# Kernel optimization log

Hardware: AMD Instinct MI355X
Metric: run time of the kernel (lower is better)

The kernel has to match this reference:

```python
import jax, jax.numpy as jnp
import numpy as np

_SAMPLING_EPS = 1e-05
_RMAX = 0.9999999403953552          # largest float32 uniform from tl.rand
_RMAX_LOG = -5.960464477539063e-08  # log(_RMAX)


def setup_inputs() -> dict:
    key = jax.random.key(0)
    k1, k2, k3, k4, k5 = jax.random.split(key, 5)
    B, V = 256, 128000
    logits = jax.random.normal(k1, (B, V), dtype=jnp.float32) * 4.0
    temperature = jax.random.uniform(k2, (B,), dtype=jnp.float32, minval=0.1, maxval=1.5)
    top_k = jax.random.randint(k3, (B,), 1, 1000).astype(jnp.int32)
    top_p = jax.random.uniform(k4, (B,), dtype=jnp.float32, minval=0.5, maxval=1.0)
    gumbel_u = jax.random.uniform(k5, (B, V), dtype=jnp.float32)
    return {
        "logits": logits,
        "temperature": temperature,
        "top_k": top_k,
        "top_p": top_p,
        "gumbel_u": gumbel_u,
        "num_logprobs": 20,
    }


def reference(logits, temperature, top_k, top_p, gumbel_u, num_logprobs):
    B, V = logits.shape
    # --- apply_temperature: divide by temp, temp<eps treated as 1.0 (greedy) ---
    temp = jnp.where(temperature < _SAMPLING_EPS, 1.0, temperature)
    logits = logits.astype(jnp.float32) / temp[:, None]

    # --- apply_top_k_top_p: sort ascending, mask, scatter back ---
    idx_sort = jnp.argsort(logits, axis=-1)                      # ascending
    logits_sort = jnp.take_along_axis(logits, idx_sort, axis=-1)
    # top-k: value of the k-th largest is at position V-k in ascending order
    k_pos = (V - top_k.astype(jnp.int32))[:, None]
    thresh = jnp.take_along_axis(logits_sort, k_pos, axis=-1)    # [B,1]
    logits_sort = jnp.where(logits_sort < thresh, -jnp.inf, logits_sort)
    # top-p: drop ascending prefix whose cumulative prob <= 1-p (keep last)
    probs_sort = jax.nn.softmax(logits_sort, axis=-1)
    cum = jnp.cumsum(probs_sort, axis=-1)
    mask_p = cum <= (1.0 - top_p)[:, None]
    mask_p = mask_p.at[:, -1].set(False)
    logits_sort = jnp.where(mask_p, -jnp.inf, logits_sort)
    # unsort back to vocab order
    inv = jnp.argsort(idx_sort, axis=-1)
    logits_f = jnp.take_along_axis(logits_sort, inv, axis=-1)

    # --- softmax + gumbel-trick sampling: argmax(p / -log(u)) ---
    probs = jax.nn.softmax(logits_f, axis=-1)
    q = -jnp.where(gumbel_u >= _RMAX, _RMAX_LOG, jnp.log(gumbel_u))
    greedy = (temperature < _SAMPLING_EPS)[:, None]  # kernel skips these rows
    ratio = jnp.where(greedy, probs, probs / q)
    sampled = jnp.argmax(ratio, axis=-1)             # [B]

    # --- gather_logprobs ---
    logprobs = jax.nn.log_softmax(logits_f, axis=-1)
    sampled_lp = jnp.take_along_axis(logprobs, sampled[:, None], axis=-1)  # [B,1]
    ranks = jnp.sum(logprobs > sampled_lp, axis=-1)                        # [B]
    topk_lp, topk_idx = jax.lax.top_k(logprobs, num_logprobs)
    indices = jnp.concatenate([sampled[:, None], topk_idx], axis=1)        # [B,1+K]
    lp_vals = jnp.concatenate([sampled_lp, topk_lp], axis=1)               # [B,1+K]

    return sampled[:, None], indices, lp_vals, ranks
```

## Files before the change

kernel.cpp:

```cpp
#include <hip/hip_runtime.h>
#include <math.h>

#define NTHR 1024
#define CAP 8192
#define BINS 4096
#define SMALL 1024
#define GUARD 16u
#define SS 4096

#define RMAX_F 0.9999999403953552f
#define RMAX_LOG_F -5.960464477539063e-08f
#define NEG_BIG -3.0e38f

__device__ __forceinline__ unsigned keyOf(float v) {
    unsigned b = __float_as_uint(v);
    return (b & 0x80000000u) ? ~b : (b | 0x80000000u);
}
__device__ __forceinline__ float valOfKey(unsigned k) {
    unsigned b = (k & 0x80000000u) ? (k ^ 0x80000000u) : ~k;
    return __uint_as_float(b);
}
__device__ __forceinline__ unsigned long long shflXor64(unsigned long long v, int m) {
    int lo = __shfl_xor((int)(unsigned)v, m);
    int hi = __shfl_xor((int)(unsigned)(v >> 32), m);
    return ((unsigned long long)(unsigned)hi << 32) | (unsigned)lo;
}

__global__ __launch_bounds__(NTHR) void sampler_kernel(
    const float* __restrict__ logits,
    const float* __restrict__ temperature,
    const int* __restrict__ top_kv,
    const float* __restrict__ top_pv,
    const float* __restrict__ gumbel,
    float* __restrict__ out,
    int B, int V, int K)
{
    const int r = blockIdx.x;
    const int tid = threadIdx.x;
    const int lane = tid & 63;
    const int wid = tid >> 6;

    __shared__ unsigned long long cand[CAP];
    __shared__ unsigned long long cand2[SMALL];
    __shared__ unsigned refHist[16 * 257];
    __shared__ int wtotI[16];
    __shared__ float varr[1024];
    __shared__ float Earr[1024];
    __shared__ float sfx[1024];
    __shared__ float sfx2[1024];
    __shared__ unsigned char flagArr[1024];
    __shared__ unsigned bitmap[64];
    __shared__ unsigned s_prefix;
    __shared__ int s_cntgt, s_total, s_lvl;
    __shared__ int s_ncand, s_nc2, s_nkeep, s_rank, s_g0, s_g1;
    __shared__ unsigned long long s_amax;
    __shared__ float s_vs;

    unsigned* hist = (unsigned*)cand;

    const float* row = logits + (long long)r * V;
    const float* urow = gumbel + (long long)r * V;

    float traw = temperature[r];
    bool greedy = traw < 1e-5f;
    float t = greedy ? 1.0f : traw;
    int k = top_kv[r];
    if (k < 1) k = 1;
    if (k > V) k = V;
    float p = top_pv[r];

    const float4* row4 = (const float4*)row;
    const int V4 = V >> 2;
    const int Vt = V4 << 2;
    const unsigned cpy = tid & 1u;

#define H4(v4) do { \
        atomicAdd(&hist[((keyOf((v4).x) >> 20) << 1) | cpy], 1u); \
        atomicAdd(&hist[((keyOf((v4).y) >> 20) << 1) | cpy], 1u); \
        atomicAdd(&hist[((keyOf((v4).z) >> 20) << 1) | cpy], 1u); \
        atomicAdd(&hist[((keyOf((v4).w) >> 20) << 1) | cpy], 1u); \
    } while (0)
#define SPEC1(val, gidx_, thr_) do { \
        float _v = (val); \
        if (_v >= (thr_)) { \
            int _pos = atomicAdd(&s_ncand, 1); \
            if (_pos < CAP) \
                cand[_pos] = ((unsigned long long)keyOf(_v) << 32) | (unsigned)(~(unsigned)(gidx_)); \
        } \
    } while (0)

    for (int i = tid; i < BINS * 2; i += NTHR) hist[i] = 0;
    __syncthreads();
    {
        int f4pos = (int)(((long long)tid * V4) >> 10);
        float4 sv = row4[f4pos];
        H4(sv);
    }
    __syncthreads();
    int ts;
    {
        int tc = 2 * k + 400;
        if (tc > 2400) tc = 2400;
        if (tc < 600) tc = 600;
        ts = (int)(((long long)tc * SS + V - 1) / V);
        if (ts < 4) ts = 4;
    }
    {
        int base = tid << 2;
        int cs = 0;
        #pragma unroll
        for (int j = 0; j < 4; ++j)
            cs += (int)(hist[(base + j) * 2] + hist[(base + j) * 2 + 1]);
        int vv = cs;
        #pragma unroll
        for (int d = 1; d < 64; d <<= 1) {
            int o = __shfl_down(vv, d);
            if (lane + d < 64) vv += o;
        }
        if (lane == 0) wtotI[wid] = vv;
        __syncthreads();
        int off = 0;
        for (int w = wid + 1; w < 16; ++w) off += wtotI[w];
        int mine = vv + off;
        int above = mine - cs;
        if (mine >= ts && above < ts) {
            int run = above;
            for (int b = base + 3; b >= base; --b) {
                int mb = (int)(hist[b * 2] + hist[b * 2 + 1]);
                if (run + mb >= ts) { s_prefix = (unsigned)b; break; }
                run += mb;
            }
        }
        if (tid == 0) s_ncand = 0;
        __syncthreads();
    }
    unsigned tlo = s_prefix << 20;
    float thrF = valOfKey(tlo);

    {
        int i = tid;
        for (; i + 3 * NTHR < V4; i += 4 * NTHR) {
            float4 a = row4[i];
            float4 b = row4[i + NTHR];
            float4 c = row4[i + 2 * NTHR];
            float4 d = row4[i + 3 * NTHR];
            SPEC1(a.x, i * 4 + 0, thrF); SPEC1(a.y, i * 4 + 1, thrF);
            SPEC1(a.z, i * 4 + 2, thrF); SPEC1(a.w, i * 4 + 3, thrF);
            SPEC1(b.x, (i + NTHR) * 4 + 0, thrF); SPEC1(b.y, (i + NTHR) * 4 + 1, thrF);
            SPEC1(b.z, (i + NTHR) * 4 + 2, thrF); SPEC1(b.w, (i + NTHR) * 4 + 3, thrF);
            SPEC1(c.x, (i + 2 * NTHR) * 4 + 0, thrF); SPEC1(c.y, (i + 2 * NTHR) * 4 + 1, thrF);
            SPEC1(c.z, (i + 2 * NTHR) * 4 + 2, thrF); SPEC1(c.w, (i + 2 * NTHR) * 4 + 3, thrF);
            SPEC1(d.x, (i + 3 * NTHR) * 4 + 0, thrF); SPEC1(d.y, (i + 3 * NTHR) * 4 + 1, thrF);
            SPEC1(d.z, (i + 3 * NTHR) * 4 + 2, thrF); SPEC1(d.w, (i + 3 * NTHR) * 4 + 3, thrF);
        }
        for (; i < V4; i += NTHR) {
            float4 a = row4[i];
            SPEC1(a.x, i * 4 + 0, thrF); SPEC1(a.y, i * 4 + 1, thrF);
            SPEC1(a.z, i * 4 + 2, thrF); SPEC1(a.w, i * 4 + 3, thrF);
        }
        for (int ii = Vt + tid; ii < V; ii += NTHR)
            SPEC1(row[ii], ii, thrF);
    }
    __syncthreads();
    int ncand = s_ncand;
    const bool fastok = (ncand >= k && ncand <= CAP);

    if (!fastok) {
        for (int i = tid; i < BINS * 2; i += NTHR) hist[i] = 0;
        __syncthreads();
        {
            int i = tid;
            for (; i + 3 * NTHR < V4; i += 4 * NTHR) {
                float4 a = row4[i];
                float4 b = row4[i + NTHR];
                float4 c = row4[i + 2 * NTHR];
                float4 d = row4[i + 3 * NTHR];
                H4(a); H4(b); H4(c); H4(d);
            }
            for (; i < V4; i += NTHR) { float4 a = row4[i]; H4(a); }
            for (int ii = Vt + tid; ii < V; ii += NTHR)
                atomicAdd(&hist[((keyOf(row[ii]) >> 20) << 1) | cpy], 1u);
        }
        __syncthreads();
        {
            int base = tid << 2;
            int cs = 0;
            #pragma unroll
            for (int j = 0; j < 4; ++j)
                cs += (int)(hist[(base + j) * 2] + hist[(base + j) * 2 + 1]);
            int vv = cs;
            #pragma unroll
            for (int d = 1; d < 64; d <<= 1) {
                int o = __shfl_down(vv, d);
                if (lane + d < 64) vv += o;
            }
            if (lane == 0) wtotI[wid] = vv;
            __syncthreads();
            int off = 0;
            for (int w = wid + 1; w < 16; ++w) off += wtotI[w];
            int mine = vv + off;
            int above = mine - cs;
            if (mine >= k && above < k) {
                int run = above;
                for (int b = base + 3; b >= base; --b) {
                    int mb = (int)(hist[b * 2] + hist[b * 2 + 1]);
                    if (run + mb >= k) {
                        s_prefix = (unsigned)b; s_cntgt = run; s_total = run + mb; s_lvl = 0;
                        break;
                    }
                    run += mb;
                }
            }
        }
        for (int level = 1; level <= 2; ++level) {
            __syncthreads();
            if (s_total <= CAP) break;
            for (int i = tid; i < 512; i += NTHR) hist[i] = 0;
            __syncthreads();
            unsigned pfx = s_prefix;
            const int msh = 32 - (12 + 8 * (level - 1));
            const int bsh = msh - 8;
            for (int i = tid; i < V4; i += NTHR) {
                float4 l4 = row4[i];
                float vv4[4] = { l4.x, l4.y, l4.z, l4.w };
                #pragma unroll
                for (int j = 0; j < 4; ++j) {
                    unsigned key = keyOf(vv4[j]);
                    if ((key >> msh) == pfx)
                        atomicAdd(&hist[(((key >> bsh) & 255u) << 1) | cpy], 1u);
                }
            }
            for (int i = Vt + tid; i < V; i += NTHR) {
                unsigned key = keyOf(row[i]);
                if ((key >> msh) == pfx)
                    atomicAdd(&hist[(((key >> bsh) & 255u) << 1) | cpy], 1u);
            }
            __syncthreads();
            if (tid == 0) {
                int run = s_cntgt;
                for (int b = 255; b >= 0; --b) {
                    int mb = (int)(hist[b * 2] + hist[b * 2 + 1]);
                    if (run + mb >= k) {
                        s_prefix = (pfx << 8) | (unsigned)b; s_cntgt = run; s_total = run + mb;
                        break;
                    }
                    run += mb;
                }
                s_lvl = level;
            }
        }
        __syncthreads();
        tlo = s_prefix << (20 - 8 * s_lvl);
        thrF = valOfKey(tlo);
        if (tid == 0) s_ncand = 0;
        __syncthreads();
        {
            int i = tid;
            for (; i + 3 * NTHR < V4; i += 4 * NTHR) {
                float4 a = row4[i];
                float4 b = row4[i + NTHR];
                float4 c = row4[i + 2 * NTHR];
                float4 d = row4[i + 3 * NTHR];
                SPEC1(a.x, i * 4 + 0, thrF); SPEC1(a.y, i * 4 + 1, thrF);
                SPEC1(a.z, i * 4 + 2, thrF); SPEC1(a.w, i * 4 + 3, thrF);
                SPEC1(b.x, (i + NTHR) * 4 + 0, thrF); SPEC1(b.y, (i + NTHR) * 4 + 1, thrF);
                SPEC1(b.z, (i + NTHR) * 4 + 2, thrF); SPEC1(b.w, (i + NTHR) * 4 + 3, thrF);
                SPEC1(c.x, (i + 2 * NTHR) * 4 + 0, thrF); SPEC1(c.y, (i + 2 * NTHR) * 4 + 1, thrF);
                SPEC1(c.z, (i + 2 * NTHR) * 4 + 2, thrF); SPEC1(c.w, (i + 2 * NTHR) * 4 + 3, thrF);
                SPEC1(d.x, (i + 3 * NTHR) * 4 + 0, thrF); SPEC1(d.y, (i + 3 * NTHR) * 4 + 1, thrF);
                SPEC1(d.z, (i + 3 * NTHR) * 4 + 2, thrF); SPEC1(d.w, (i + 3 * NTHR) * 4 + 3, thrF);
            }
            for (; i < V4; i += NTHR) {
                float4 a = row4[i];
                SPEC1(a.x, i * 4 + 0, thrF); SPEC1(a.y, i * 4 + 1, thrF);
                SPEC1(a.z, i * 4 + 2, thrF); SPEC1(a.w, i * 4 + 3, thrF);
            }
            for (int ii = Vt + tid; ii < V; ii += NTHR)
                SPEC1(row[ii], ii, thrF);
        }
        __syncthreads();
        ncand = s_ncand;
        if (ncand > CAP) ncand = CAP;
        if (k > ncand) k = ncand;
    }
    if (k > ncand) k = ncand;

    bool fromC2 = false;
    bool bigSort = false;
    if (ncand > SMALL) {
        unsigned pfx; int run; int bb;
        if (fastok) { pfx = 0u; run = 0; bb = 32; }
        else { pfx = s_prefix; run = s_cntgt; bb = 20 - 8 * s_lvl; }
        int totR = ncand;
        while (totR > SMALL - 16 && bb > 0) {
            int step = (bb >= 8) ? 8 : bb;
            bb -= step;
            int nbins = 1 << step;
            for (int i = tid; i < 16 * 257; i += NTHR) refHist[i] = 0;
            __syncthreads();
            {
                const int sh = bb + step;
                const unsigned lc = (unsigned)(lane & 15) * 257u;
                for (int i = tid; i < ncand; i += NTHR) {
                    unsigned key = (unsigned)(cand[i] >> 32);
                    bool in = (sh >= 32) || ((key >> sh) == pfx);
                    if (in)
                        atomicAdd(&refHist[lc + ((key >> bb) & (unsigned)(nbins - 1))], 1u);
                }
            }
            __syncthreads();
            int cnt = 0;
            if (tid < 256 && tid < nbins) {
                #pragma unroll
                for (int c = 0; c < 16; ++c) cnt += (int)refHist[c * 257 + tid];
            }
            int vv = cnt;
            #pragma unroll
            for (int d = 1; d < 64; d <<= 1) {
                int o = __shfl_down(vv, d);
                if (lane + d < 64) vv += o;
            }
            if (tid < 256 && lane == 0) wtotI[wid] = vv;
            __syncthreads();
            if (tid < 256) {
                int off = 0;
                for (int w = wid + 1; w < 4; ++w) off += wtotI[w];
                int incl = vv + off;
                int abv = incl - cnt;
                int kk = k - run;
                if (incl >= kk && abv < kk) {
                    s_prefix = (pfx << step) | (unsigned)tid;
                    s_cntgt = run + abv;
                    s_total = run + abv + cnt;
                }
            }
            __syncthreads();
            pfx = s_prefix;
            run = s_cntgt;
            totR = s_total;
        }
        unsigned tref0 = (bb > 0) ? (pfx << bb) : pfx;
        unsigned tref = (tref0 >= GUARD) ? (tref0 - GUARD) : 0u;
        if (tid == 0) s_nc2 = 0;
        __syncthreads();
        for (int i = tid; i < ncand; i += NTHR) {
            unsigned long long cv = cand[i];
            bool pred = ((unsigned)(cv >> 32) >= tref);
            unsigned long long mask = __ballot(pred ? 1 : 0);
            if (mask) {
                int leader = __ffsll(mask) - 1;
                int cnt2 = __popcll(mask);
                int bpos = 0;
                if (lane == leader) bpos = atomicAdd(&s_nc2, cnt2);
                bpos = __shfl(bpos, leader);
                if (pred) {
                    int pos = bpos + __popcll(mask & ((1ULL << lane) - 1ULL));
                    if (pos < SMALL) cand2[pos] = cv;
                }
            }
        }
        __syncthreads();
        int nc2 = s_nc2;
        if (nc2 <= SMALL) { ncand = nc2; fromC2 = true; }
        else bigSort = true;
    }

    if (!bigSort) {
        const unsigned long long* src = fromC2 ? cand2 : cand;
        unsigned long long v = (tid < ncand) ? src[tid] : 0ULL;
        int seg = 0;
        #pragma unroll
        for (int size = 2; size <= SMALL; size <<= 1) {
            #pragma unroll
            for (int stride = size >> 1; stride > 0; stride >>= 1) {
                unsigned long long o;
                if (stride < 64) {
                    o = shflXor64(v, stride);
                } else {
                    cand[seg * SMALL + tid] = v;
                    __syncthreads();
                    o = cand[seg * SMALL + (tid ^ stride)];
                    seg ^= 1;
                }
                bool takeMax = (((tid & size) == 0) == ((tid & stride) == 0));
                unsigned long long mx = (v > o) ? v : o;
                unsigned long long mn = (v > o) ? o : v;
                v = takeMax ? mx : mn;
            }
        }
        cand[tid] = v;
        varr[tid] = (tid < ncand) ? (valOfKey((unsigned)(v >> 32)) / t) : NEG_BIG;
        __syncthreads();
    } else {
        int P = 2; while (P < ncand) P <<= 1;
        for (int i = ncand + tid; i < P; i += NTHR) cand[i] = 0ULL;
        __syncthreads();
        for (int size = 2; size <= P; size <<= 1) {
            for (int stride = size >> 1; stride > 0; stride >>= 1) {
                for (int i = tid; i < P; i += NTHR) {
                    int j = i ^ stride;
                    if (j > i) {
                        unsigned long long a = cand[i], b = cand[j];
                        bool up = ((i & size) == 0);
                        bool sw = up ? (a < b) : (a > b);
                        if (sw) { cand[i] = b; cand[j] = a; }
                    }
                }
                __syncthreads();
            }
        }
        for (int i = tid; i < 1024; i += NTHR)
            varr[i] = (i < ncand) ? (valOfKey((unsigned)(cand[i] >> 32)) / t) : NEG_BIG;
        __syncthreads();
    }

    const float m = varr[0];
    const float tkeyV = varr[k - 1];
    int ntop = k;
    while (ntop < ncand) {
        float vi = (ntop < 1024) ? varr[ntop]
                                 : (valOfKey((unsigned)(cand[ntop] >> 32)) / t);
        if (vi != tkeyV) break;
        ++ntop;
    }
    if (ntop > 1024) ntop = 1024;

    {
        float e = (tid < ntop) ? expf(varr[tid] - m) : 0.0f;
        Earr[tid] = e;
        sfx[tid] = e;
        if (tid == 0) { s_nkeep = 0; s_rank = 0; s_amax = 0ULL; }
        if (tid < 64) bitmap[tid] = 0;
    }
    __syncthreads();
    {
        float* A = sfx;
        float* Bf = sfx2;
        #pragma unroll
        for (int d = 1; d < 1024; d <<= 1) {
            float t0 = (tid + d < 1024) ? A[tid + d] : 0.0f;
            Bf[tid] = A[tid] + t0;
            __syncthreads();
            float* tmp = A; A = Bf; Bf = tmp;
        }
    }
    const float Zp = sfx[0];
    const float cmp = 1.0f - p;
    {
        int local = 0;
        for (int i = tid; i < ntop; i += NTHR)
            if (sfx[i] / Zp > cmp) local++;
        #pragma unroll
        for (int d = 1; d < 64; d <<= 1) local += __shfl_xor(local, d);
        if (lane == 0 && local) atomicAdd(&s_nkeep, local);
    }
    __syncthreads();
    const int nkeep = s_nkeep;
    if (tid == 0) {
        float vb = varr[nkeep - 1];
        int g0 = nkeep - 1;
        while (g0 > 0 && varr[g0 - 1] == vb) --g0;
        int g1 = nkeep;
        while (g1 < ntop && varr[g1] == vb) ++g1;
        s_g0 = g0; s_g1 = g1;
    }
    __syncthreads();
    const int g0 = s_g0, g1 = s_g1;
    const int mkeep = nkeep - g0;
    for (int i = g0 + tid; i < g1; i += NTHR) {
        unsigned gi = ~(unsigned)(cand[i] & 0xFFFFFFFFull);
        int rk = 0;
        for (int j = g0; j < g1; ++j) {
            unsigned gj = ~(unsigned)(cand[j] & 0xFFFFFFFFull);
            if (gj > gi) rk++;
        }
        flagArr[i] = (rk < mkeep) ? 1 : 0;
    }
    __syncthreads();

    const float Z2 = (nkeep < 1024) ? (Zp - sfx[nkeep]) : Zp;
    const float L = logf(Z2);

    {
        unsigned long long lm = 0ULL;
        for (int i = tid; i < g1; i += NTHR) {
            if (i < g0 || flagArr[i]) {
                unsigned lo = (unsigned)(cand[i] & 0xFFFFFFFFull);
                unsigned gidx = ~lo;
                float u = urow[gidx];
                float q = -((u >= RMAX_F) ? RMAX_LOG_F : logf(u));
                float prob = Earr[i] / Z2;
                float ratio = greedy ? prob : (prob / q);
                unsigned long long comp = ((unsigned long long)__float_as_uint(ratio) << 32) | lo;
                if (comp > lm) lm = comp;
                if (gidx < 2048) atomicOr(&bitmap[gidx >> 5], 1u << (gidx & 31));
            }
        }
        #pragma unroll
        for (int d = 1; d < 64; d <<= 1) {
            unsigned long long o = shflXor64(lm, d);
            if (o > lm) lm = o;
        }
        if (lane == 0 && lm) atomicMax(&s_amax, lm);
    }
    __syncthreads();
    const unsigned samp_lo = (unsigned)(s_amax & 0xFFFFFFFFull);
    const unsigned samp = ~samp_lo;
    for (int i = tid; i < ntop; i += NTHR)
        if ((unsigned)(cand[i] & 0xFFFFFFFFull) == samp_lo) s_vs = varr[i];
    __syncthreads();
    const float lp_s = (s_vs - m) - L;
    {
        int local = 0;
        for (int i = tid; i < nkeep; i += NTHR)
            if ((varr[i] - m) - L > lp_s) local++;
        #pragma unroll
        for (int d = 1; d < 64; d <<= 1) local += __shfl_xor(local, d);
        if (lane == 0 && local) atomicAdd(&s_rank, local);
    }
    __syncthreads();

    float* o_samp = out;
    float* o_idx  = out + B;
    float* o_lp   = out + B + (long long)B * (K + 1);
    float* o_rank = out + B + 2LL * B * (K + 1);
    const long long rowo = (long long)r * (K + 1);
    const int ntk = (nkeep < K) ? nkeep : K;

    if (tid < g1) {
        const int i = tid;
        bool kept = (i < g0) || flagArr[i];
        if (kept) {
            float v = varr[i];
            int rs, re, base;
            if (i >= g0) { rs = g0; re = g1; base = g0; }
            else {
                rs = i; while (rs > 0 && varr[rs - 1] == v) --rs;
                re = i + 1; while (re < g1 && varr[re] == v) ++re;
                base = rs;
            }
            if (base < ntk) {
                unsigned myidx = ~(unsigned)(cand[i] & 0xFFFFFFFFull);
                int cnt = 0;
                for (int j = rs; j < re; ++j) {
                    if (j == i) continue;
                    if (j >= g0 && !flagArr[j]) continue;
                    unsigned gj = ~(unsigned)(cand[j] & 0xFFFFFFFFull);
                    if (gj < myidx) cnt++;
                }
                int slot = base + cnt;
                if (slot < ntk) {
                    o_idx[rowo + 1 + slot] = (float)myidx;
                    o_lp[rowo + 1 + slot] = (v - m) - L;
                }
            }
        }
    }

    if (tid == 0) {
        o_samp[r] = (float)samp;
        o_idx[rowo] = (float)samp;
        o_lp[rowo] = lp_s;
        o_rank[r] = (float)s_rank;
        if (nkeep < K) {
            int j = 0;
            for (int c = nkeep; c < K; ++c) {
                while (bitmap[j >> 5] & (1u << (j & 31))) ++j;
                o_idx[rowo + 1 + c] = (float)j;
                o_lp[rowo + 1 + c] = NEG_BIG;
                ++j;
            }
        }
    }
}

extern "C" void kernel_launch(void* const* d_in, const int* in_sizes, int n_in,
                              void* d_out, int out_size, void* d_ws, size_t ws_size,
                              hipStream_t stream) {
    const float* logits      = (const float*)d_in[0];
    const float* temperature = (const float*)d_in[1];
    const int*   top_k       = (const int*)d_in[2];
    const float* top_p       = (const float*)d_in[3];
    const float* gumbel      = (const float*)d_in[4];
    int B = in_sizes[1];
    int V = in_sizes[0] / B;
    int K = (out_size / B - 4) / 2;
    sampler_kernel<<<B, NTHR, 0, stream>>>(logits, temperature, top_k, top_p,
                                           gumbel, (float*)d_out, B, V, K);
}
```

Measured before the change: 265.4 us.

## Split sampler into threshold, multi-block compaction, and tail kernels via workspace

Breaks the single per-row kernel into three launches. One estimates the candidate threshold from a sample, the next compacts candidates with four 256-thread blocks per row using global atomics into a workspace, and the last loads those candidates into LDS to finish selection and sampling. The aim is more parallelism in the full-row scan, which was bound to one 1024-thread block per row with very large LDS use and therefore low occupancy. In exchange it adds launch overhead, global atomics and a workspace round-trip, and it needs a large workspace (B*8192*8 bytes); if that is not provided, it falls back to the old single-kernel path.

New measurement: 622.8 us. +134.6%, slower.

```diff
diff --git a/kernel.cpp b/kernel.cpp
--- a/kernel.cpp
+++ b/kernel.cpp
@@ -7,10 +7,14 @@
 #define SMALL 1024
 #define GUARD 16u
 #define SS 4096
+#define NS 4
+#define ATHR 256
 
 #define RMAX_F 0.9999999403953552f
 #define RMAX_LOG_F -5.960464477539063e-08f
 #define NEG_BIG -3.0e38f
+
+typedef unsigned long long ull;
 
 __device__ __forceinline__ unsigned keyOf(float v) {
     unsigned b = __float_as_uint(v);
@@ -20,28 +24,167 @@
     unsigned b = (k & 0x80000000u) ? (k ^ 0x80000000u) : ~k;
     return __uint_as_float(b);
 }
-__device__ __forceinline__ unsigned long long shflXor64(unsigned long long v, int m) {
+__device__ __forceinline__ ull shflXor64(ull v, int m) {
     int lo = __shfl_xor((int)(unsigned)v, m);
     int hi = __shfl_xor((int)(unsigned)(v >> 32), m);
-    return ((unsigned long long)(unsigned)hi << 32) | (unsigned)lo;
+    return ((ull)(unsigned)hi << 32) | (unsigned)lo;
 }
 
-__global__ __launch_bounds__(NTHR) void sampler_kernel(
+
+#define H4(v4) do { \
+        atomicAdd(&hist[((keyOf((v4).x) >> 20) << 1) | cpy], 1u); \
+        atomicAdd(&hist[((keyOf((v4).y) >> 20) << 1) | cpy], 1u); \
+        atomicAdd(&hist[((keyOf((v4).z) >> 20) << 1) | cpy], 1u); \
+        atomicAdd(&hist[((keyOf((v4).w) >> 20) << 1) | cpy], 1u); \
+    } while (0)
+
+__global__ __launch_bounds__(NTHR) void a0_thresh(
+    const float* __restrict__ logits,
+    const int* __restrict__ top_kv,
+    int* __restrict__ ws_cnt,
+    unsigned* __restrict__ ws_tlo,
+    int B, int V)
+{
+    const int r = blockIdx.x;
+    const int tid = threadIdx.x;
+    const int lane = tid & 63;
+    const int wid = tid >> 6;
+    __shared__ unsigned hist[BINS * 2];
+    __shared__ int wtotI[16];
+    __shared__ unsigned s_prefix;
+
+    const float* row = logits + (long long)r * V;
+    const float4* row4 = (const float4*)row;
+    const int V4 = V >> 2;
+    const unsigned cpy = tid & 1u;
+
+    int k = top_kv[r];
+    if (k < 1) k = 1;
+    if (k > V) k = V;
+
+    for (int i = tid; i < BINS * 2; i += NTHR) hist[i] = 0;
+    __syncthreads();
+    {
+        int f4pos = (int)(((long long)tid * V4) >> 10);
+        float4 sv = row4[f4pos];
+        H4(sv);
+    }
+    __syncthreads();
+    int ts;
+    {
+        int tc = 2 * k + 400;
+        if (tc > 2400) tc = 2400;
+        if (tc < 600) tc = 600;
+        ts = (int)(((long long)tc * SS + V - 1) / V);
+        if (ts < 4) ts = 4;
+    }
+    {
+        int base = tid << 2;
+        int cs = 0;
+        #pragma unroll
+        for (int j = 0; j < 4; ++j)
+            cs += (int)(hist[(base + j) * 2] + hist[(base + j) * 2 + 1]);
+        int vv = cs;
+        #pragma unroll
+        for (int d = 1; d < 64; d <<= 1) {
+            int o = __shfl_down(vv, d);
+            if (lane + d < 64) vv += o;
+        }
+        if (lane == 0) wtotI[wid] = vv;
+        __syncthreads();
+        int off = 0;
+        for (int w = wid + 1; w < 16; ++w) off += wtotI[w];
+        int mine = vv + off;
+        int above = mine - cs;
+        if (mine >= ts && above < ts) {
+            int run = above;
+            for (int b = base + 3; b >= base; --b) {
+                int mb = (int)(hist[b * 2] + hist[b * 2 + 1]);
+                if (run + mb >= ts) { s_prefix = (unsigned)b; break; }
+                run += mb;
+            }
+        }
+    }
+    __syncthreads();
+    if (tid == 0) {
+        ws_tlo[r] = s_prefix << 20;
+        ws_cnt[r] = 0;
+    }
+}
+
+__global__ __launch_bounds__(ATHR) void a1_compact(
+    const float* __restrict__ logits,
+    const unsigned* __restrict__ ws_tlo,
+    int* __restrict__ ws_cnt,
+    ull* __restrict__ ws_cand,
+    int B, int V)
+{
+    const int r = blockIdx.x / NS;
+    const int s = blockIdx.x % NS;
+    const int tid = threadIdx.x;
+
+    const float* row = logits + (long long)r * V;
+    const float4* row4 = (const float4*)row;
+    const int V4 = V >> 2;
+    const int Vt = V4 << 2;
+    const float thrF = valOfKey(ws_tlo[r]);
+    int* cnt = ws_cnt + r;
+    ull* wc = ws_cand + (size_t)r * CAP;
+
+#define SPECG(val, gidx_) do { \
+        float _v = (val); \
+        if (_v >= thrF) { \
+            int _pos = atomicAdd(cnt, 1); \
+            if (_pos < CAP) \
+                wc[_pos] = ((ull)keyOf(_v) << 32) | (unsigned)(~(unsigned)(gidx_)); \
+        } \
+    } while (0)
+
+    const int q0 = (int)(((long long)s * V4) / NS);
+    const int q1 = (int)(((long long)(s + 1) * V4) / NS);
+    int i = q0 + tid;
+    for (; i + 3 * ATHR < q1; i += 4 * ATHR) {
+        float4 a = row4[i];
+        float4 b = row4[i + ATHR];
+        float4 c = row4[i + 2 * ATHR];
+        float4 d = row4[i + 3 * ATHR];
+        SPECG(a.x, i * 4 + 0); SPECG(a.y, i * 4 + 1);
+        SPECG(a.z, i * 4 + 2); SPECG(a.w, i * 4 + 3);
+        SPECG(b.x, (i + ATHR) * 4 + 0); SPECG(b.y, (i + ATHR) * 4 + 1);
+        SPECG(b.z, (i + ATHR) * 4 + 2); SPECG(b.w, (i + ATHR) * 4 + 3);
+        SPECG(c.x, (i + 2 * ATHR) * 4 + 0); SPECG(c.y, (i + 2 * ATHR) * 4 + 1);
+        SPECG(c.z, (i + 2 * ATHR) * 4 + 2); SPECG(c.w, (i + 2 * ATHR) * 4 + 3);
+        SPECG(d.x, (i + 3 * ATHR) * 4 + 0); SPECG(d.y, (i + 3 * ATHR) * 4 + 1);
+        SPECG(d.z, (i + 3 * ATHR) * 4 + 2); SPECG(d.w, (i + 3 * ATHR) * 4 + 3);
+    }
+    for (; i < q1; i += ATHR) {
+        float4 a = row4[i];
+        SPECG(a.x, i * 4 + 0); SPECG(a.y, i * 4 + 1);
+        SPECG(a.z, i * 4 + 2); SPECG(a.w, i * 4 + 3);
+    }
+    if (s == NS - 1)
+        for (int ii = Vt + tid; ii < V; ii += ATHR)
+            SPECG(row[ii], ii);
+}
+
+__global__ __launch_bounds__(NTHR) void sampler_tail(
     const float* __restrict__ logits,
     const float* __restrict__ temperature,
     const int* __restrict__ top_kv,
     const float* __restrict__ top_pv,
     const float* __restrict__ gumbel,
     float* __restrict__ out,
-    int B, int V, int K)
+    const int* __restrict__ ws_cnt,
+    const ull* __restrict__ ws_cand,
+    int B, int V, int K, int use_ws)
 {
     const int r = blockIdx.x;
     const int tid = threadIdx.x;
     const int lane = tid & 63;
     const int wid = tid >> 6;
 
-    __shared__ unsigned long long cand[CAP];
-    __shared__ unsigned long long cand2[SMALL];
+    __shared__ ull cand[CAP];
+    __shared__ ull cand2[SMALL];
     __shared__ unsigned refHist[16 * 257];
     __shared__ int wtotI[16];
     __shared__ float varr[1024];
@@ -53,7 +196,7 @@
     __shared__ unsigned s_prefix;
     __shared__ int s_cntgt, s_total, s_lvl;
     __shared__ int s_ncand, s_nc2, s_nkeep, s_rank, s_g0, s_g1;
-    __shared__ unsigned long long s_amax;
+    __shared__ ull s_amax;
     __shared__ float s_vs;
 
     unsigned* hist = (unsigned*)cand;
@@ -74,114 +217,48 @@
     const int Vt = V4 << 2;
     const unsigned cpy = tid & 1u;
 
-#define H4(v4) do { \
-        atomicAdd(&hist[((keyOf((v4).x) >> 20) << 1) | cpy], 1u); \
-        atomicAdd(&hist[((keyOf((v4).y) >> 20) << 1) | cpy], 1u); \
-        atomicAdd(&hist[((keyOf((v4).z) >> 20) << 1) | cpy], 1u); \
-        atomicAdd(&hist[((keyOf((v4).w) >> 20) << 1) | cpy], 1u); \
-    } while (0)
 #define SPEC1(val, gidx_, thr_) do { \
         float _v = (val); \
         if (_v >= (thr_)) { \
             int _pos = atomicAdd(&s_ncand, 1); \
             if (_pos < CAP) \
-                cand[_pos] = ((unsigned long long)keyOf(_v) << 32) | (unsigned)(~(unsigned)(gidx_)); \
+                cand[_pos] = ((ull)keyOf(_v) << 32) | (unsigned)(~(unsigned)(gidx_)); \
         } \
     } while (0)
 
-    for (int i = tid; i < BINS * 2; i += NTHR) hist[i] = 0;
-    __syncthreads();
-    {
-        int f4pos = (int)(((long long)tid * V4) >> 10);
-        float4 sv = row4[f4pos];
-        H4(sv);
-    }
-    __syncthreads();
-    int ts;
-    {
-        int tc = 2 * k + 400;
-        if (tc > 2400) tc = 2400;
-        if (tc < 600) tc = 600;
-        ts = (int)(((long long)tc * SS + V - 1) / V);
-        if (ts < 4) ts = 4;
-    }
-    {
-        int base = tid << 2;
-        int cs = 0;
-        #pragma unroll
-        for (int j = 0; j < 4; ++j)
-            cs += (int)(hist[(base + j) * 2] + hist[(base + j) * 2 + 1]);
-        int vv = cs;
-        #pragma unroll
-        for (int d = 1; d < 64; d <<= 1) {
-            int o = __shfl_down(vv, d);
-            if (lane + d < 64) vv += o;
-        }
-        if (lane == 0) wtotI[wid] = vv;
-        __syncthreads();
-        int off = 0;
-        for (int w = wid + 1; w < 16; ++w) off += wtotI[w];
-        int mine = vv + off;
-        int above = mine - cs;
-        if (mine >= ts && above < ts) {
-            int run = above;
-            for (int b = base + 3; b >= base; --b) {
-                int mb = (int)(hist[b * 2] + hist[b * 2 + 1]);
-                if (run + mb >= ts) { s_prefix = (unsigned)b; break; }
-                run += mb;
-            }
-        }
-        if (tid == 0) s_ncand = 0;
-        __syncthreads();
-    }
-    unsigned tlo = s_prefix << 20;
-    float thrF = valOfKey(tlo);
-
-    {
-        int i = tid;
-        for (; i + 3 * NTHR < V4; i += 4 * NTHR) {
-            float4 a = row4[i];
-            float4 b = row4[i + NTHR];
-            float4 c = row4[i + 2 * NTHR];
-            float4 d = row4[i + 3 * NTHR];
-            SPEC1(a.x, i * 4 + 0, thrF); SPEC1(a.y, i * 4 + 1, thrF);
-            SPEC1(a.z, i * 4 + 2, thrF); SPEC1(a.w, i * 4 + 3, thrF);
-            SPEC1(b.x, (i + NTHR) * 4 + 0, thrF); SPEC1(b.y, (i + NTHR) * 4 + 1, thrF);
-            SPEC1(b.z, (i + NTHR) * 4 + 2, thrF); SPEC1(b.w, (i + NTHR) * 4 + 3, thrF);
-            SPEC1(c.x, (i + 2 * NTHR) * 4 + 0, thrF); SPEC1(c.y, (i + 2 * NTHR) * 4 + 1, thrF);
-            SPEC1(c.z, (i + 2 * NTHR) * 4 + 2, thrF); SPEC1(c.w, (i + 2 * NTHR) * 4 + 3, thrF);
-            SPEC1(d.x, (i + 3 * NTHR) * 4 + 0, thrF); SPEC1(d.y, (i + 3 * NTHR) * 4 + 1, thrF);
-            SPEC1(d.z, (i + 3 * NTHR) * 4 + 2, thrF); SPEC1(d.w, (i + 3 * NTHR) * 4 + 3, thrF);
-        }
-        for (; i < V4; i += NTHR) {
-            float4 a = row4[i];
-            SPEC1(a.x, i * 4 + 0, thrF); SPEC1(a.y, i * 4 + 1, thrF);
-            SPEC1(a.z, i * 4 + 2, thrF); SPEC1(a.w, i * 4 + 3, thrF);
-        }
-        for (int ii = Vt + tid; ii < V; ii += NTHR)
-            SPEC1(row[ii], ii, thrF);
-    }
-    __syncthreads();
-    int ncand = s_ncand;
-    const bool fastok = (ncand >= k && ncand <= CAP);
-
-    if (!fastok) {
+    int ncand = 0;
+    bool fastok = false;
+    bool haveCand = false;
+
+    if (use_ws) {
+        int nc = ws_cnt[r];
+        if (nc >= k && nc <= CAP) {
+            const ull* wc = ws_cand + (size_t)r * CAP;
+            for (int i = tid; i < nc; i += NTHR) cand[i] = wc[i];
+            __syncthreads();
+            ncand = nc;
+            fastok = true;
+            haveCand = true;
+        }
+    }
+
+    if (!haveCand) {
         for (int i = tid; i < BINS * 2; i += NTHR) hist[i] = 0;
         __syncthreads();
         {
-            int i = tid;
-            for (; i + 3 * NTHR < V4; i += 4 * NTHR) {
-                float4 a = row4[i];
-                float4 b = row4[i + NTHR];
-                float4 c = row4[i + 2 * NTHR];
-                float4 d = row4[i + 3 * NTHR];
-                H4(a); H4(b); H4(c); H4(d);
-            }
-            for (; i < V4; i += NTHR) { float4 a = row4[i]; H4(a); }
-            for (int ii = Vt + tid; ii < V; ii += NTHR)
-                atomicAdd(&hist[((keyOf(row[ii]) >> 20) << 1) | cpy], 1u);
-        }
-        __syncthreads();
+            int f4pos = (int)(((long long)tid * V4) >> 10);
+            float4 sv = row4[f4pos];
+            H4(sv);
+        }
+        __syncthreads();
+        int ts;
+        {
+            int tc = 2 * k + 400;
+            if (tc > 2400) tc = 2400;
+            if (tc < 600) tc = 600;
+            ts = (int)(((long long)tc * SS + V - 1) / V);
+            if (ts < 4) ts = 4;
+        }
         {
             int base = tid << 2;
             int cs = 0;
@@ -200,60 +277,20 @@
             for (int w = wid + 1; w < 16; ++w) off += wtotI[w];
             int mine = vv + off;
             int above = mine - cs;
-            if (mine >= k && above < k) {
+            if (mine >= ts && above < ts) {
                 int run = above;
                 for (int b = base + 3; b >= base; --b) {
                     int mb = (int)(hist[b * 2] + hist[b * 2 + 1]);
-                    if (run + mb >= k) {
-                        s_prefix = (unsigned)b; s_cntgt = run; s_total = run + mb; s_lvl = 0;
-                        break;
-                    }
+                    if (run + mb >= ts) { s_prefix = (unsigned)b; break; }
                     run += mb;
                 }
             }
-        }
-        for (int level = 1; level <= 2; ++level) {
-            __syncthreads();
-            if (s_total <= CAP) break;
-            for (int i = tid; i < 512; i += NTHR) hist[i] = 0;
-            __syncthreads();
-            unsigned pfx = s_prefix;
-            const int msh = 32 - (12 + 8 * (level - 1));
-            const int bsh = msh - 8;
-            for (int i = tid; i < V4; i += NTHR) {
-                float4 l4 = row4[i];
-                float vv4[4] = { l4.x, l4.y, l4.z, l4.w };
-                #pragma unroll
-                for (int j = 0; j < 4; ++j) {
-                    unsigned key = keyOf(vv4[j]);
-                    if ((key >> msh) == pfx)
-                        atomicAdd(&hist[(((key >> bsh) & 255u) << 1) | cpy], 1u);
-                }
-            }
-            for (int i = Vt + tid; i < V; i += NTHR) {
-                unsigned key = keyOf(row[i]);
-                if ((key >> msh) == pfx)
-                    atomicAdd(&hist[(((key >> bsh) & 255u) << 1) | cpy], 1u);
-            }
-            __syncthreads();
-            if (tid == 0) {
-                int run = s_cntgt;
-                for (int b = 255; b >= 0; --b) {
-                    int mb = (int)(hist[b * 2] + hist[b * 2 + 1]);
-                    if (run + mb >= k) {
-                        s_prefix = (pfx << 8) | (unsigned)b; s_cntgt = run; s_total = run + mb;
-                        break;
-                    }
-                    run += mb;
-                }
-                s_lvl = level;
-            }
-        }
-        __syncthreads();
-        tlo = s_prefix << (20 - 8 * s_lvl);
-        thrF = valOfKey(tlo);
-        if (tid == 0) s_ncand = 0;
-        __syncthreads();
+            if (tid == 0) s_ncand = 0;
+            __syncthreads();
+        }
+        unsigned tlo = s_prefix << 20;
+        float thrF = valOfKey(tlo);
+
         {
             int i = tid;
             for (; i + 3 * NTHR < V4; i += 4 * NTHR) {
@@ -280,8 +317,126 @@
         }
         __syncthreads();
         ncand = s_ncand;
-        if (ncand > CAP) ncand = CAP;
-        if (k > ncand) k = ncand;
+        fastok = (ncand >= k && ncand <= CAP);
+
+        if (!fastok) {
+            for (int i = tid; i < BINS * 2; i += NTHR) hist[i] = 0;
+            __syncthreads();
+            {
+                int i = tid;
+                for (; i + 3 * NTHR < V4; i += 4 * NTHR) {
+                    float4 a = row4[i];
+                    float4 b = row4[i + NTHR];
+                    float4 c = row4[i + 2 * NTHR];
+                    float4 d = row4[i + 3 * NTHR];
+                    H4(a); H4(b); H4(c); H4(d);
+                }
+                for (; i < V4; i += NTHR) { float4 a = row4[i]; H4(a); }
+                for (int ii = Vt + tid; ii < V; ii += NTHR)
+                    atomicAdd(&hist[((keyOf(row[ii]) >> 20) << 1) | cpy], 1u);
+            }
+            __syncthreads();
+            {
+                int base = tid << 2;
+                int cs = 0;
+                #pragma unroll
+                for (int j = 0; j < 4; ++j)
+                    cs += (int)(hist[(base + j) * 2] + hist[(base + j) * 2 + 1]);
+                int vv = cs;
+                #pragma unroll
+                for (int d = 1; d < 64; d <<= 1) {
+                    int o = __shfl_down(vv, d);
+                    if (lane + d < 64) vv += o;
+                }
+                if (lane == 0) wtotI[wid] = vv;
+                __syncthreads();
+                int off = 0;
+                for (int w = wid + 1; w < 16; ++w) off += wtotI[w];
+                int mine = vv + off;
+                int above = mine - cs;
+                if (mine >= k && above < k) {
+                    int run = above;
+                    for (int b = base + 3; b >= base; --b) {
+                        int mb = (int)(hist[b * 2] + hist[b * 2 + 1]);
+                        if (run + mb >= k) {
+                            s_prefix = (unsigned)b; s_cntgt = run; s_total = run + mb; s_lvl = 0;
+                            break;
+                        }
+                        run += mb;
+                    }
+                }
+            }
+            for (int level = 1; level <= 2; ++level) {
+                __syncthreads();
+                if (s_total <= CAP) break;
+                for (int i = tid; i < 512; i += NTHR) hist[i] = 0;
+                __syncthreads();
+                unsigned pfx = s_prefix;
+                const int msh = 32 - (12 + 8 * (level - 1));
+                const int bsh = msh - 8;
+                for (int i = tid; i < V4; i += NTHR) {
+                    float4 l4 = row4[i];
+                    float vv4[4] = { l4.x, l4.y, l4.z, l4.w };
+                    #pragma unroll
+                    for (int j = 0; j < 4; ++j) {
+                        unsigned key = keyOf(vv4[j]);
+                        if ((key >> msh) == pfx)
+                            atomicAdd(&hist[(((key >> bsh) & 255u) << 1) | cpy], 1u);
+                    }
+                }
+                for (int i = Vt + tid; i < V; i += NTHR) {
+                    unsigned key = keyOf(row[i]);
+                    if ((key >> msh) == pfx)
+                        atomicAdd(&hist[(((key >> bsh) & 255u) << 1) | cpy], 1u);
+                }
+                __syncthreads();
+                if (tid == 0) {
+                    int run = s_cntgt;
+                    for (int b = 255; b >= 0; --b) {
+                        int mb = (int)(hist[b * 2] + hist[b * 2 + 1]);
+                        if (run + mb >= k) {
+                            s_prefix = (pfx << 8) | (unsigned)b; s_cntgt = run; s_total = run + mb;
+                            break;
+                        }
+                        run += mb;
+                    }
+                    s_lvl = level;
+                }
+            }
+            __syncthreads();
+            unsigned tlo2 = s_prefix << (20 - 8 * s_lvl);
+            float thrF2 = valOfKey(tlo2);
+            if (tid == 0) s_ncand = 0;
+            __syncthreads();
+            {
+                int i = tid;
+                for (; i + 3 * NTHR < V4; i += 4 * NTHR) {
+                    float4 a = row4[i];
+                    float4 b = row4[i + NTHR];
+                    float4 c = row4[i + 2 * NTHR];
+                    float4 d = row4[i + 3 * NTHR];
+                    SPEC1(a.x, i * 4 + 0, thrF2); SPEC1(a.y, i * 4 + 1, thrF2);
+                    SPEC1(a.z, i * 4 + 2, thrF2); SPEC1(a.w, i * 4 + 3, thrF2);
+                    SPEC1(b.x, (i + NTHR) * 4 + 0, thrF2); SPEC1(b.y, (i + NTHR) * 4 + 1, thrF2);
+                    SPEC1(b.z, (i + NTHR) * 4 + 2, thrF2); SPEC1(b.w, (i + NTHR) * 4 + 3, thrF2);
+                    SPEC1(c.x, (i + 2 * NTHR) * 4 + 0, thrF2); SPEC1(c.y, (i + 2 * NTHR) * 4 + 1, thrF2);
+                    SPEC1(c.z, (i + 2 * NTHR) * 4 + 2, thrF2); SPEC1(c.w, (i + 2 * NTHR) * 4 + 3, thrF2);
+                    SPEC1(d.x, (i + 3 * NTHR) * 4 + 0, thrF2); SPEC1(d.y, (i + 3 * NTHR) * 4 + 1, thrF2);
+                    SPEC1(d.z, (i + 3 * NTHR) * 4 + 2, thrF2); SPEC1(d.w, (i + 3 * NTHR) * 4 + 3, thrF2);
+                }
+                for (; i < V4; i += NTHR) {
+                    float4 a = row4[i];
+                    SPEC1(a.x, i * 4 + 0, thrF2); SPEC1(a.y, i * 4 + 1, thrF2);
+                    SPEC1(a.z, i * 4 + 2, thrF2); SPEC1(a.w, i * 4 + 3, thrF2);
+                }
+                for (int ii = Vt + tid; ii < V; ii += NTHR)
+                    SPEC1(row[ii], ii, thrF2);
+            }
+            __syncthreads();
+            ncand = s_ncand;
+            if (ncand > CAP) ncand = CAP;
+            if (k > ncand) k = ncand;
+        }
     }
     if (k > ncand) k = ncand;
 
@@ -344,9 +499,9 @@
         if (tid == 0) s_nc2 = 0;
         __syncthreads();
         for (int i = tid; i < ncand; i += NTHR) {
-            unsigned long long cv = cand[i];
+            ull cv = cand[i];
             bool pred = ((unsigned)(cv >> 32) >= tref);
-            unsigned long long mask = __ballot(pred ? 1 : 0);
+            ull mask = __ballot(pred ? 1 : 0);
             if (mask) {
                 int leader = __ffsll(mask) - 1;
                 int cnt2 = __popcll(mask);
@@ -366,14 +521,14 @@
     }
 
     if (!bigSort) {
-        const unsigned long long* src = fromC2 ? cand2 : cand;
-        unsigned long long v = (tid < ncand) ? src[tid] : 0ULL;
+        const ull* src = fromC2 ? cand2 : cand;
+        ull v = (tid < ncand) ? src[tid] : 0ULL;
         int seg = 0;
         #pragma unroll
         for (int size = 2; size <= SMALL; size <<= 1) {
             #pragma unroll
             for (int stride = size >> 1; stride > 0; stride >>= 1) {
-                unsigned long long o;
+                ull o;
                 if (stride < 64) {
                     o = shflXor64(v, stride);
                 } else {
@@ -383,8 +538,8 @@
                     seg ^= 1;
                 }
                 bool takeMax = (((tid & size) == 0) == ((tid & stride) == 0));
-                unsigned long long mx = (v > o) ? v : o;
-                unsigned long long mn = (v > o) ? o : v;
+                ull mx = (v > o) ? v : o;
+                ull mn = (v > o) ? o : v;
                 v = takeMax ? mx : mn;
             }
         }
@@ -400,7 +555,7 @@
                 for (int i = tid; i < P; i += NTHR) {
                     int j = i ^ stride;
                     if (j > i) {
-                        unsigned long long a = cand[i], b = cand[j];
+                        ull a = cand[i], b = cand[j];
                         bool up = ((i & size) == 0);
                         bool sw = up ? (a < b) : (a > b);
                         if (sw) { cand[i] = b; cand[j] = a; }
@@ -482,7 +637,7 @@
     const float L = logf(Z2);
 
     {
-        unsigned long long lm = 0ULL;
+        ull lm = 0ULL;
         for (int i = tid; i < g1; i += NTHR) {
             if (i < g0 || flagArr[i]) {
                 unsigned lo = (unsigned)(cand[i] & 0xFFFFFFFFull);
@@ -491,14 +646,14 @@
                 float q = -((u >= RMAX_F) ? RMAX_LOG_F : logf(u));
                 float prob = Earr[i] / Z2;
                 float ratio = greedy ? prob : (prob / q);
-                unsigned long long comp = ((unsigned long long)__float_as_uint(ratio) << 32) | lo;
+                ull comp = ((ull)__float_as_uint(ratio) << 32) | lo;
                 if (comp > lm) lm = comp;
                 if (gidx < 2048) atomicOr(&bitmap[gidx >> 5], 1u << (gidx & 31));
             }
         }
         #pragma unroll
         for (int d = 1; d < 64; d <<= 1) {
-            unsigned long long o = shflXor64(lm, d);
+            ull o = shflXor64(lm, d);
             if (o > lm) lm = o;
         }
         if (lane == 0 && lm) atomicMax(&s_amax, lm);
@@ -585,6 +740,22 @@
     int B = in_sizes[1];
     int V = in_sizes[0] / B;
     int K = (out_size / B - 4) / 2;
-    sampler_kernel<<<B, NTHR, 0, stream>>>(logits, temperature, top_k, top_p,
-                                           gumbel, (float*)d_out, B, V, K);
+
+    size_t off = ((size_t)B * 8 + 255) & ~(size_t)255;
+    size_t need = off + (size_t)B * CAP * sizeof(ull);
+
+    if (d_ws != nullptr && ws_size >= need) {
+        int* ws_cnt = (int*)d_ws;
+        unsigned* ws_tlo = (unsigned*)((char*)d_ws + (size_t)B * 4);
+        ull* ws_cand = (ull*)((char*)d_ws + off);
+        a0_thresh<<<B, NTHR, 0, stream>>>(logits, top_k, ws_cnt, ws_tlo, B, V);
+        a1_compact<<<B * NS, ATHR, 0, stream>>>(logits, ws_tlo, ws_cnt, ws_cand, B, V);
+        sampler_tail<<<B, NTHR, 0, stream>>>(logits, temperature, top_k, top_p,
+                                             gumbel, (float*)d_out, ws_cnt, ws_cand,
+                                             B, V, K, 1);
+    } else {
+        sampler_tail<<<B, NTHR, 0, stream>>>(logits, temperature, top_k, top_p,
+                                             gumbel, (float*)d_out, nullptr, nullptr,
+                                             B, V, K, 0);
+    }
 }
```
